# Kernel optimization log

Measured on AMD Instinct MI355X. Metric: run time of the kernel, lower is better.

Reference implementation:

```python
import jax, jax.numpy as jnp
import numpy as np

D_MODEL = 256
D_STATE = 16
D_CONV = 3
D_INNER = 256          # expand=1
D_HALF = D_INNER // 2  # 128
DT_RANK = 16           # ceil(256/16)
B, L0, L1 = 4, 4096, 4096


def setup_inputs() -> dict:
    key = jax.random.key(0)
    ks = jax.random.split(key, 10)
    u_0 = jax.random.normal(ks[0], (B, L0, D_MODEL), jnp.float32)
    u_1 = jax.random.normal(ks[1], (B, L1, D_MODEL), jnp.float32)
    in_proj_w = jax.random.normal(ks[2], (D_INNER, D_MODEL), jnp.float32) * (D_MODEL ** -0.5)
    conv_x_w = jax.random.normal(ks[3], (D_HALF, 1, D_CONV), jnp.float32) * (D_CONV ** -0.5)
    conv_z_w = jax.random.normal(ks[4], (D_HALF, 1, D_CONV), jnp.float32) * (D_CONV ** -0.5)
    x_proj_w = jax.random.normal(ks[5], (DT_RANK + 2 * D_STATE, D_HALF), jnp.float32) * (D_HALF ** -0.5)
    dt_init_std = DT_RANK ** -0.5
    dt_proj_w = jax.random.uniform(ks[6], (D_HALF, DT_RANK), jnp.float32, -dt_init_std, dt_init_std)
    # dt bias = inverse-softplus of dt ~ LogUniform(1e-3, 1e-1)
    dt = jnp.exp(jax.random.uniform(ks[7], (D_HALF,), jnp.float32) * (np.log(0.1) - np.log(0.001)) + np.log(0.001))
    dt = jnp.clip(dt, 1e-4, None)
    dt_proj_b = dt + jnp.log(-jnp.expm1(-dt))
    A_log = jnp.log(jnp.broadcast_to(jnp.arange(1, D_STATE + 1, dtype=jnp.float32), (D_HALF, D_STATE)))
    D_param = jnp.ones((D_HALF,), jnp.float32)
    out_proj_w = jax.random.normal(ks[8], (D_MODEL, D_INNER), jnp.float32) * (D_INNER ** -0.5)
    return {"u_0": u_0, "u_1": u_1, "in_proj_w": in_proj_w, "conv_x_w": conv_x_w,
            "conv_z_w": conv_z_w, "x_proj_w": x_proj_w, "dt_proj_w": dt_proj_w,
            "dt_proj_b": dt_proj_b, "A_log": A_log, "D": D_param, "out_proj_w": out_proj_w}


def _dwconv(x, w):
    # x: [B, C, L], w: [C, 1, K] depthwise, padding='same', no bias (conv_bias//2 == 0)
    return jax.lax.conv_general_dilated(
        x, w, window_strides=(1,), padding='SAME',
        feature_group_count=x.shape[1], dimension_numbers=('NCH', 'OIH', 'NCH'))


def _selective_scan(u, delta, A, Bm, Cm, Dv):
    # u, delta: [B, L, d]; A: [d, n]; Bm, Cm: [B, L, n]; Dv: [d]
    dA = jnp.exp(delta[..., None] * A)                       # [B, L, d, n]
    dBu = (delta * u)[..., None] * Bm[:, :, None, :]         # [B, L, d, n]
    def combine(c1, c2):
        a1, b1 = c1
        a2, b2 = c2
        return a2 * a1, a2 * b1 + b2
    _, h = jax.lax.associative_scan(combine, (dA, dBu), axis=1)  # h: [B, L, d, n]
    return jnp.einsum('bldn,bln->bld', h, Cm) + u * Dv


def _stream(u, in_proj_w, conv_x_w, conv_z_w, x_proj_w, dt_proj_w, dt_proj_b, A, D, out_proj_w):
    xz = jnp.einsum('bld,ed->ble', u, in_proj_w)             # [B, L, d_inner]
    x, z = jnp.split(xz, 2, axis=-1)                         # [B, L, d_half] each
    x = jnp.swapaxes(x, 1, 2)                                # [B, d_half, L]
    z = jnp.swapaxes(z, 1, 2)
    x_f = jax.nn.silu(_dwconv(x, conv_x_w))
    z_f = jax.nn.silu(_dwconv(z, conv_z_w))
    xf = jnp.swapaxes(x_f, 1, 2)                             # [B, L, d_half]
    dbl = jnp.einsum('bld,ed->ble', xf, x_proj_w)            # [B, L, dt_rank + 2n]
    dt, Bm, Cm = jnp.split(dbl, [DT_RANK, DT_RANK + D_STATE], axis=-1)
    dt = jnp.einsum('blr,dr->bld', dt, dt_proj_w)
    delta = jax.nn.softplus(dt + dt_proj_b)                  # delta_bias + delta_softplus
    y = _selective_scan(xf, delta, A, Bm, Cm, D)             # [B, L, d_half]
    cat = jnp.concatenate([y, jnp.swapaxes(z_f, 1, 2)], axis=-1)  # [B, L, d_inner]
    return jnp.einsum('ble,oe->blo', cat, out_proj_w)


def reference(u_0, u_1, in_proj_w, conv_x_w, conv_z_w, x_proj_w, dt_proj_w, dt_proj_b, A_log, D, out_proj_w):
    A = -jnp.exp(A_log)
    out0 = _stream(u_0, in_proj_w, conv_x_w, conv_z_w, x_proj_w, dt_proj_w, dt_proj_b, A, D, out_proj_w)
    out1 = _stream(u_1, in_proj_w, conv_x_w, conv_z_w, x_proj_w, dt_proj_w, dt_proj_b, A, D, out_proj_w)
    return (out0, out1)
```

## Files before the change

kernel.cpp:

```cpp
#include <hip/hip_runtime.h>
#include <hip/hip_bf16.h>
#include <cstdint>

#define DEV __device__ __forceinline__

typedef __attribute__((ext_vector_type(8))) short short8;
typedef __attribute__((ext_vector_type(4))) float f32x4;
typedef __attribute__((ext_vector_type(4))) unsigned short us4;
typedef __attribute__((ext_vector_type(8))) unsigned short us8;

DEV unsigned short f2bf(float x) {
    unsigned int u = __float_as_uint(x);
    unsigned int r = (u + 0x7FFFu + ((u >> 16) & 1u)) >> 16;
    return (unsigned short)r;
}
DEV float bf2f(unsigned short h) { return __uint_as_float(((unsigned int)h) << 16); }

DEV void gld_lds16(const unsigned short* g, unsigned short* l) {
    __builtin_amdgcn_global_load_lds(
        (const __attribute__((address_space(1))) unsigned int*)g,
        (__attribute__((address_space(3))) unsigned int*)l, 16, 0, 0);
}

#define LL 4096
#define DM 256
#define DH 128
#define SB_TOT 8
#define CH1 32
#define NCH 128
#define LOG2E 1.44269504088896f

__global__ __launch_bounds__(256) void prep_kernel(
    const float* __restrict__ u0, const float* __restrict__ u1,
    const float* __restrict__ inw, const float* __restrict__ outw,
    const float* __restrict__ xpw, const float* __restrict__ dtw,
    unsigned short* __restrict__ ubf, unsigned short* __restrict__ wbi,
    unsigned short* __restrict__ wbo, unsigned short* __restrict__ Wb)
{
    int gid = blockIdx.x * 256 + threadIdx.x;
    int i = gid * 4;
    if (i < 4194304) {
        f32x4 v = *(const f32x4*)&u0[i];
        us4 r = { f2bf(v.x), f2bf(v.y), f2bf(v.z), f2bf(v.w) };
        *(us4*)&ubf[i] = r;
    } else if (i < 8388608) {
        int j = i - 4194304;
        f32x4 v = *(const f32x4*)&u1[j];
        us4 r = { f2bf(v.x), f2bf(v.y), f2bf(v.z), f2bf(v.w) };
        *(us4*)&ubf[4194304 + j] = r;
    } else if (i < 8454144) {
        int j = i - 8388608;
        f32x4 v = *(const f32x4*)&inw[j];
        us4 r = { f2bf(v.x), f2bf(v.y), f2bf(v.z), f2bf(v.w) };
        *(us4*)&wbi[j] = r;
    } else if (i < 8519680) {
        int j = i - 8454144;
        f32x4 v = *(const f32x4*)&outw[j];
        us4 r = { f2bf(v.x), f2bf(v.y), f2bf(v.z), f2bf(v.w) };
        *(us4*)&wbo[j] = r;
    } else if (i < 8540160) {
        int j = i - 8519680;
        int n = j >> 7, k0 = j & 127;
        if (n < 128) {
            float a0 = 0.f, a1 = 0.f, a2 = 0.f, a3 = 0.f;
            const float* dw = dtw + n * 16;
            #pragma unroll
            for (int r = 0; r < 16; ++r) {
                float w = dw[r];
                const float* xr = xpw + r * 128 + k0;
                a0 = fmaf(w, xr[0], a0);
                a1 = fmaf(w, xr[1], a1);
                a2 = fmaf(w, xr[2], a2);
                a3 = fmaf(w, xr[3], a3);
            }
            us4 rr = { f2bf(a0), f2bf(a1), f2bf(a2), f2bf(a3) };
            *(us4*)&Wb[n * 128 + k0] = rr;
        } else {
            f32x4 v = *(const f32x4*)&xpw[(n - 112) * 128 + k0];
            us4 rr = { f2bf(v.x), f2bf(v.y), f2bf(v.z), f2bf(v.w) };
            *(us4*)&Wb[n * 128 + k0] = rr;
        }
    }
}

template<int F32OUT>
__global__ __launch_bounds__(256) void gemm_bt(
    const unsigned short* __restrict__ A, const unsigned short* __restrict__ B,
    float* __restrict__ Cf, unsigned short* __restrict__ Cb)
{
    __shared__ __align__(16) unsigned short As[128 * 32];
    __shared__ __align__(16) unsigned short Bs[128 * 32];
    const int t = threadIdx.x;
    const int m0 = blockIdx.x * 128, n0 = blockIdx.y * 128;
    const int lane = t & 63, wv = t >> 6;
    const int wm = (wv & 1) * 64, wn = (wv >> 1) * 64;
    const int lr = lane & 15, lk = (lane >> 4) * 8;
    const int srow = lane >> 2, scol = (lane & 3) * 8;

    f32x4 acc[4][4] = {};
    for (int kt = 0; kt < 8; ++kt) {
        const int k0 = kt * 32;
        #pragma unroll
        for (int h = 0; h < 2; ++h) {
            const int c = wv + h * 4;
            const unsigned short* ga = A + (size_t)(m0 + c * 16 + srow) * 256 + k0 + scol;
            const unsigned short* gb = B + (size_t)(n0 + c * 16 + srow) * 256 + k0 + scol;
            gld_lds16(ga, &As[c * 512]);
            gld_lds16(gb, &Bs[c * 512]);
        }
        __syncthreads();
        short8 av[4], bv[4];
        #pragma unroll
        for (int i = 0; i < 4; ++i) av[i] = *(const short8*)&As[(wm + i * 16 + lr) * 32 + lk];
        #pragma unroll
        for (int i = 0; i < 4; ++i) bv[i] = *(const short8*)&Bs[(wn + i * 16 + lr) * 32 + lk];
        #pragma unroll
        for (int i = 0; i < 4; ++i)
            #pragma unroll
            for (int j = 0; j < 4; ++j)
                acc[i][j] = __builtin_amdgcn_mfma_f32_16x16x32_bf16(av[i], bv[j], acc[i][j], 0, 0, 0);
        __syncthreads();
    }
    #pragma unroll
    for (int i = 0; i < 4; ++i) {
        #pragma unroll
        for (int j = 0; j < 4; ++j) {
            int r0 = m0 + wm + i * 16 + (lane >> 4) * 4;
            int cc = n0 + wn + j * 16 + lr;
            #pragma unroll
            for (int r = 0; r < 4; ++r) {
                float v = acc[i][j][r];
                if (F32OUT) Cf[(size_t)(r0 + r) * 256 + cc] = v;
                else        Cb[(size_t)(r0 + r) * 256 + cc] = f2bf(v);
            }
        }
    }
}

template<int FUSE_SCAN>
__global__ __launch_bounds__(256) void convproj_k(
    const unsigned short* __restrict__ xz, const unsigned short* __restrict__ Wb,
    const float* __restrict__ wx, const float* __restrict__ wz,
    const float* __restrict__ dtb, const float* __restrict__ alog,
    float* __restrict__ xf, unsigned short* __restrict__ catb,
    float* __restrict__ delta, float* __restrict__ BC,
    float* __restrict__ P, float* __restrict__ H)
{
    __shared__ __align__(16) unsigned short As[64 * 136];
    __shared__ float bc_s[64 * 16];
    const int t = threadIdx.x;
    const int m0 = blockIdx.x * 64;
    #pragma unroll
    for (int i = 0; i < 8; ++i) {
        int s = t + i * 256;
        int r = s >> 5, g = s & 31;
        int gr = m0 + r;
        int l = gr & 4095;
        int c; const float* wp; const unsigned short* bp;
        if (g < 16) { c = g * 8;        wp = wx; bp = xz + (size_t)gr * 256 + c; }
        else        { c = (g - 16) * 8; wp = wz; bp = xz + (size_t)gr * 256 + 128 + c; }
        us8 zz = (us8)0;
        us8 vm = (l > 0)    ? *(const us8*)(bp - 256) : zz;
        us8 v0 = *(const us8*)bp;
        us8 vp = (l < 4095) ? *(const us8*)(bp + 256) : zz;
        float o[8];
        #pragma unroll
        for (int j = 0; j < 8; ++j) {
            int cc = c + j;
            float v = bf2f(vm[j]) * wp[cc * 3] + bf2f(v0[j]) * wp[cc * 3 + 1]
                    + bf2f(vp[j]) * wp[cc * 3 + 2];
            v = v / (1.f + __expf(-v));
            o[j] = v;
        }
        us8 rb8 = { f2bf(o[0]), f2bf(o[1]), f2bf(o[2]), f2bf(o[3]),
                    f2bf(o[4]), f2bf(o[5]), f2bf(o[6]), f2bf(o[7]) };
        if (g < 16) {
            *(us8*)&As[r * 136 + c] = rb8;
            *(f32x4*)&xf[(size_t)gr * 128 + c]     = *(f32x4*)&o[0];
            *(f32x4*)&xf[(size_t)gr * 128 + c + 4] = *(f32x4*)&o[4];
        } else {
            *(us8*)&catb[(size_t)gr * 256 + 128 + c] = rb8;
        }
    }
    __syncthreads();
    const int lane = t & 63, wv = t >> 6;
    const int lr = lane & 15, lk = (lane >> 4) * 8;
    f32x4 acc[10] = {};
    #pragma unroll
    for (int kt = 0; kt < 4; ++kt) {
        const int k0 = kt * 32;
        short8 av = *(const short8*)&As[(wv * 16 + lr) * 136 + k0 + lk];
        #pragma unroll
        for (int j = 0; j < 10; ++j) {
            short8 bv = *(const short8*)(Wb + (j * 16 + lr) * 128 + k0 + lk);
            acc[j] = __builtin_amdgcn_mfma_f32_16x16x32_bf16(av, bv, acc[j], 0, 0, 0);
        }
    }
    const int r0 = (lane >> 4) * 4;
    #pragma unroll
    for (int j = 0; j < 10; ++j) {
        int col = j * 16 + lr;
        #pragma unroll
        for (int r = 0; r < 4; ++r) {
            float v = acc[j][r];
            int lrow = wv * 16 + r0 + r;
            size_t row = (size_t)m0 + lrow;
            if (j < 8) {
                float x = v + dtb[col];
                float sp = (x > 20.f) ? x : __logf(1.f + __expf(x));
                delta[row * 128 + col] = sp;
            } else {
                BC[row * 32 + (col - 128)] = v;
                if (FUSE_SCAN && j == 8) bc_s[lrow * 16 + lr] = v;
            }
        }
    }
    if (!FUSE_SCAN) return;

    __syncthreads();
    const int hh = t >> 7, tl = t & 127;
    const int sb = m0 >> 12;
    const int ch = ((m0 & 4095) >> 5) + hh;
    const size_t rb = (size_t)m0 + hh * 32;
    float Ar[16];
    #pragma unroll
    for (int n = 0; n < 16; ++n) Ar[n] = -__expf(alog[tl * 16 + n]) * LOG2E;
    float h[16], p[16];
    #pragma unroll
    for (int n = 0; n < 16; ++n) { h[n] = 0.f; p[n] = 1.f; }
    for (int i = 0; i < CH1; ++i) {
        float dt = delta[(rb + i) * DH + tl];
        float uu = xf[(rb + i) * DH + tl];
        float du = dt * uu;
        float bl[16];
        *(f32x4*)&bl[0]  = *(const f32x4*)&bc_s[(hh * 32 + i) * 16];
        *(f32x4*)&bl[4]  = *(const f32x4*)&bc_s[(hh * 32 + i) * 16 + 4];
        *(f32x4*)&bl[8]  = *(const f32x4*)&bc_s[(hh * 32 + i) * 16 + 8];
        *(f32x4*)&bl[12] = *(const f32x4*)&bc_s[(hh * 32 + i) * 16 + 12];
        #pragma unroll
        for (int n = 0; n < 16; ++n) {
            float a = exp2f(dt * Ar[n]);
            h[n] = fmaf(a, h[n], du * bl[n]);
            p[n] *= a;
        }
    }
    size_t ob = (((size_t)sb * NCH + ch) * 128 + tl) * 16;
    #pragma unroll
    for (int n4 = 0; n4 < 16; n4 += 4) {
        f32x4 pv = { p[n4], p[n4 + 1], p[n4 + 2], p[n4 + 3] };
        f32x4 hv = { h[n4], h[n4 + 1], h[n4 + 2], h[n4 + 3] };
        *(f32x4*)&P[ob + n4] = pv;
        *(f32x4*)&H[ob + n4] = hv;
    }
}

__global__ __launch_bounds__(128) void scan_p1(
    const float* __restrict__ delta, const float* __restrict__ xf,
    const float* __restrict__ BC, const float* __restrict__ alog,
    float* __restrict__ P, float* __restrict__ H)
{
    __shared__ float dt_s[CH1 * 128];
    __shared__ float du_s[CH1 * 128];
    __shared__ float b_s[CH1 * 16];
    int t = threadIdx.x;
    int ch = blockIdx.x, sb = blockIdx.y;
    size_t rb = (size_t)sb * LL + (size_t)ch * CH1;
    for (int q = t; q < CH1 * 32; q += 128) {
        int row = q >> 5, c4 = (q & 31) * 4;
        f32x4 dv = *(const f32x4*)&delta[(rb + row) * DH + c4];
        f32x4 uv = *(const f32x4*)&xf[(rb + row) * DH + c4];
        *(f32x4*)&dt_s[row * 128 + c4] = dv;
        f32x4 duv = dv * uv;
        *(f32x4*)&du_s[row * 128 + c4] = duv;
    }
    {
        int q = t & 127;
        int row = q >> 2, c4 = (q & 3) * 4;
        *(f32x4*)&b_s[row * 16 + c4] = *(const f32x4*)&BC[(rb + row) * 32 + c4];
    }
    __syncthreads();
    float Ar[16];
    #pragma unroll
    for (int n = 0; n < 16; ++n) Ar[n] = -__expf(alog[t * 16 + n]) * LOG2E;
    float h[16], p[16];
    #pragma unroll
    for (int n = 0; n < 16; ++n) { h[n] = 0.f; p[n] = 1.f; }
    for (int i = 0; i < CH1; ++i) {
        float dt = dt_s[i * 128 + t];
        float du = du_s[i * 128 + t];
        float bl[16];
        *(f32x4*)&bl[0]  = *(const f32x4*)&b_s[i * 16];
        *(f32x4*)&bl[4]  = *(const f32x4*)&b_s[i * 16 + 4];
        *(f32x4*)&bl[8]  = *(const f32x4*)&b_s[i * 16 + 8];
        *(f32x4*)&bl[12] = *(const f32x4*)&b_s[i * 16 + 12];
        #pragma unroll
        for (int n = 0; n < 16; ++n) {
            float a = exp2f(dt * Ar[n]);
            h[n] = fmaf(a, h[n], du * bl[n]);
            p[n] *= a;
        }
    }
    size_t ob = (((size_t)sb * NCH + ch) * 128 + t) * 16;
    #pragma unroll
    for (int n4 = 0; n4 < 16; n4 += 4) {
        f32x4 pv = { p[n4], p[n4 + 1], p[n4 + 2], p[n4 + 3] };
        f32x4 hv = { h[n4], h[n4 + 1], h[n4 + 2], h[n4 + 3] };
        *(f32x4*)&P[ob + n4] = pv;
        *(f32x4*)&H[ob + n4] = hv;
    }
}

__global__ __launch_bounds__(256) void scan_p2(const float* __restrict__ P, float* __restrict__ H)
{
    __shared__ float Ps[NCH * 16], Hs[NCH * 16];
    int t = threadIdx.x;
    int d = blockIdx.x, sb = blockIdx.y;
    for (int q = t; q < NCH * 4; q += 256) {
        int ch = q >> 2, c4 = (q & 3) * 4;
        size_t g = (((size_t)sb * NCH + ch) * 128 + d) * 16 + c4;
        *(f32x4*)&Ps[ch * 16 + c4] = *(const f32x4*)&P[g];
        *(f32x4*)&Hs[ch * 16 + c4] = *(const f32x4*)&H[g];
    }
    __syncthreads();
    if (t < 16) {
        float hin = 0.f;
        for (int c = 0; c < NCH; ++c) {
            float pp = Ps[c * 16 + t], hl = Hs[c * 16 + t];
            Hs[c * 16 + t] = hin;
            hin = fmaf(pp, hin, hl);
        }
    }
    __syncthreads();
    for (int q = t; q < NCH * 4; q += 256) {
        int ch = q >> 2, c4 = (q & 3) * 4;
        size_t g = (((size_t)sb * NCH + ch) * 128 + d) * 16 + c4;
        *(f32x4*)&H[g] = *(const f32x4*)&Hs[ch * 16 + c4];
    }
}

__global__ __launch_bounds__(128) void scan_p3(
    const float* __restrict__ delta, const float* __restrict__ xf,
    const float* __restrict__ BC, const float* __restrict__ alog,
    const float* __restrict__ Dp, const float* __restrict__ H,
    unsigned short* __restrict__ catb)
{
    __shared__ float dt_s[CH1 * 128];
    __shared__ float u_s[CH1 * 128];
    __shared__ float b_s[CH1 * 16];
    __shared__ float c_s[CH1 * 16];
    int t = threadIdx.x;
    int ch = blockIdx.x, sb = blockIdx.y;
    size_t rb = (size_t)sb * LL + (size_t)ch * CH1;
    for (int q = t; q < CH1 * 32; q += 128) {
        int row = q >> 5, c4 = (q & 31) * 4;
        *(f32x4*)&dt_s[row * 128 + c4] = *(const f32x4*)&delta[(rb + row) * DH + c4];
        *(f32x4*)&u_s[row * 128 + c4]  = *(const f32x4*)&xf[(rb + row) * DH + c4];
    }
    {
        int q = t & 127;
        int row = q >> 2, c4 = (q & 3) * 4;
        *(f32x4*)&b_s[row * 16 + c4] = *(const f32x4*)&BC[(rb + row) * 32 + c4];
        *(f32x4*)&c_s[row * 16 + c4] = *(const f32x4*)&BC[(rb + row) * 32 + 16 + c4];
    }
    __syncthreads();
    float Ar[16];
    #pragma unroll
    for (int n = 0; n < 16; ++n) Ar[n] = -__expf(alog[t * 16 + n]) * LOG2E;
    float Dv = Dp[t];
    size_t ob = (((size_t)sb * NCH + ch) * 128 + t) * 16;
    float h[16];
    #pragma unroll
    for (int n4 = 0; n4 < 16; n4 += 4) {
        f32x4 hv = *(const f32x4*)&H[ob + n4];
        h[n4] = hv.x; h[n4 + 1] = hv.y; h[n4 + 2] = hv.z; h[n4 + 3] = hv.w;
    }
    for (int i = 0; i < CH1; ++i) {
        float dt = dt_s[i * 128 + t];
        float uu = u_s[i * 128 + t];
        float du = dt * uu;
        float bl[16], cl[16];
        *(f32x4*)&bl[0]  = *(const f32x4*)&b_s[i * 16];
        *(f32x4*)&bl[4]  = *(const f32x4*)&b_s[i * 16 + 4];
        *(f32x4*)&bl[8]  = *(const f32x4*)&b_s[i * 16 + 8];
        *(f32x4*)&bl[12] = *(const f32x4*)&b_s[i * 16 + 12];
        *(f32x4*)&cl[0]  = *(const f32x4*)&c_s[i * 16];
        *(f32x4*)&cl[4]  = *(const f32x4*)&c_s[i * 16 + 4];
        *(f32x4*)&cl[8]  = *(const f32x4*)&c_s[i * 16 + 8];
        *(f32x4*)&cl[12] = *(const f32x4*)&c_s[i * 16 + 12];
        float y0 = uu * Dv, y1 = 0.f, y2 = 0.f, y3 = 0.f;
        #pragma unroll
        for (int n = 0; n < 16; n += 4) {
            float a0 = exp2f(dt * Ar[n]);
            float a1 = exp2f(dt * Ar[n + 1]);
            float a2 = exp2f(dt * Ar[n + 2]);
            float a3 = exp2f(dt * Ar[n + 3]);
            h[n]     = fmaf(a0, h[n],     du * bl[n]);
            h[n + 1] = fmaf(a1, h[n + 1], du * bl[n + 1]);
            h[n + 2] = fmaf(a2, h[n + 2], du * bl[n + 2]);
            h[n + 3] = fmaf(a3, h[n + 3], du * bl[n + 3]);
            y0 = fmaf(h[n],     cl[n],     y0);
            y1 = fmaf(h[n + 1], cl[n + 1], y1);
            y2 = fmaf(h[n + 2], cl[n + 2], y2);
            y3 = fmaf(h[n + 3], cl[n + 3], y3);
        }
        float y = (y0 + y1) + (y2 + y3);
        catb[(rb + i) * DM + t] = f2bf(y);
    }
}

extern "C" void kernel_launch(void* const* d_in, const int* in_sizes, int n_in,
                              void* d_out, int out_size, void* d_ws, size_t ws_size,
                              hipStream_t stream) {
    const float* u0   = (const float*)d_in[0];
    const float* u1   = (const float*)d_in[1];
    const float* inw  = (const float*)d_in[2];
    const float* cxw  = (const float*)d_in[3];
    const float* czw  = (const float*)d_in[4];
    const float* xpw  = (const float*)d_in[5];
    const float* dtw  = (const float*)d_in[6];
    const float* dtb  = (const float*)d_in[7];
    const float* alog = (const float*)d_in[8];
    const float* Dp   = (const float*)d_in[9];
    const float* outw = (const float*)d_in[10];

    char* ws = (char*)d_ws;
    unsigned short* ubf  = (unsigned short*)(ws + 0);
    float* delta         = (float*)(ws + 0);
    unsigned short* xzbf = (unsigned short*)(ws + 16777216);
    float* P_a           = (float*)(ws + 16777216);
    float* H_a           = (float*)(ws + 25165824);
    float* xf            = (float*)(ws + 33554432);
    float* BC            = (float*)(ws + 50331648);
    unsigned short* catb = (unsigned short*)(ws + 54525952);
    unsigned short* wbi  = (unsigned short*)(ws + 71303168);
    unsigned short* wbo  = (unsigned short*)(ws + 71434240);
    unsigned short* Wb   = (unsigned short*)(ws + 71565312);
    float* P_f           = (float*)(ws + 71606272);
    float* H_f           = (float*)(ws + 79994880);

    float* outp = (float*)d_out;

    prep_kernel<<<8340, 256, 0, stream>>>(u0, u1, inw, outw, xpw, dtw, ubf, wbi, wbo, Wb);
    gemm_bt<0><<<dim3(256, 2), 256, 0, stream>>>(ubf, wbi, nullptr, xzbf);

    if (ws_size >= 88383488ull) {
        convproj_k<1><<<512, 256, 0, stream>>>(xzbf, Wb, cxw, czw, dtb, alog,
                                               xf, catb, delta, BC, P_f, H_f);
        scan_p2<<<dim3(128, 8), 256, 0, stream>>>(P_f, H_f);
        scan_p3<<<dim3(NCH, 8), 128, 0, stream>>>(delta, xf, BC, alog, Dp, H_f, catb);
    } else {
        convproj_k<0><<<512, 256, 0, stream>>>(xzbf, Wb, cxw, czw, dtb, alog,
                                               xf, catb, delta, BC, nullptr, nullptr);
        scan_p1<<<dim3(NCH, 8), 128, 0, stream>>>(delta, xf, BC, alog, P_a, H_a);
        scan_p2<<<dim3(128, 8), 256, 0, stream>>>(P_a, H_a);
        scan_p3<<<dim3(NCH, 8), 128, 0, stream>>>(delta, xf, BC, alog, Dp, H_a, catb);
    }
    gemm_bt<1><<<dim3(256, 2), 256, 0, stream>>>(catb, wbo, outp, nullptr);
}
```

Measured before the change: 212.2 us.

## Halve convproj tile to 32 rows, split scan states across halves, drop LDS staging

convproj_k now handles 32 rows per block over 1024 blocks, with a remapped block-to-row order. The four waves split the 10 MFMA column tiles between two row tiles. In the fused scan, the two 128-thread halves now each own 8 of the 16 states for the same chunk instead of separate chunks, and delta for the chunk is preloaded into registers. scan_p1 and scan_p3 drop the LDS staging of delta and xf in favour of direct per-thread global loads plus a 32-entry register array. The aim is more parallelism and occupancy, less LDS use and shorter serial scan chains, at the cost of redundant delta/xf reads across halves and more register pressure.

```diff
diff --git a/kernel.cpp b/kernel.cpp
--- a/kernel.cpp
+++ b/kernel.cpp
@@ -146,12 +146,14 @@
     float* __restrict__ delta, float* __restrict__ BC,
     float* __restrict__ P, float* __restrict__ H)
 {
-    __shared__ __align__(16) unsigned short As[64 * 136];
-    __shared__ float bc_s[64 * 16];
+    __shared__ __align__(16) unsigned short As[32 * 136];
+    __shared__ float bc_s[32 * 16];
     const int t = threadIdx.x;
-    const int m0 = blockIdx.x * 64;
-    #pragma unroll
-    for (int i = 0; i < 8; ++i) {
+    const int kk = blockIdx.x & 7, yy = blockIdx.x >> 3;
+    const int m0 = (4 * kk + (yy & 3) + 32 * (yy >> 2)) * 32;
+
+    #pragma unroll
+    for (int i = 0; i < 4; ++i) {
         int s = t + i * 256;
         int r = s >> 5, g = s & 31;
         int gr = m0 + r;
@@ -185,33 +187,36 @@
     __syncthreads();
     const int lane = t & 63, wv = t >> 6;
     const int lr = lane & 15, lk = (lane >> 4) * 8;
-    f32x4 acc[10] = {};
+    const int rt = (wv & 1) * 16;
+    const int jbase = (wv >> 1) * 5;
+    f32x4 acc[5] = {};
     #pragma unroll
     for (int kt = 0; kt < 4; ++kt) {
         const int k0 = kt * 32;
-        short8 av = *(const short8*)&As[(wv * 16 + lr) * 136 + k0 + lk];
-        #pragma unroll
-        for (int j = 0; j < 10; ++j) {
-            short8 bv = *(const short8*)(Wb + (j * 16 + lr) * 128 + k0 + lk);
+        short8 av = *(const short8*)&As[(rt + lr) * 136 + k0 + lk];
+        #pragma unroll
+        for (int j = 0; j < 5; ++j) {
+            short8 bv = *(const short8*)(Wb + ((jbase + j) * 16 + lr) * 128 + k0 + lk);
             acc[j] = __builtin_amdgcn_mfma_f32_16x16x32_bf16(av, bv, acc[j], 0, 0, 0);
         }
     }
     const int r0 = (lane >> 4) * 4;
     #pragma unroll
-    for (int j = 0; j < 10; ++j) {
-        int col = j * 16 + lr;
+    for (int j = 0; j < 5; ++j) {
+        int jj = jbase + j;
+        int col = jj * 16 + lr;
         #pragma unroll
         for (int r = 0; r < 4; ++r) {
             float v = acc[j][r];
-            int lrow = wv * 16 + r0 + r;
+            int lrow = rt + r0 + r;
             size_t row = (size_t)m0 + lrow;
-            if (j < 8) {
+            if (jj < 8) {
                 float x = v + dtb[col];
                 float sp = (x > 20.f) ? x : __logf(1.f + __expf(x));
                 delta[row * 128 + col] = sp;
             } else {
                 BC[row * 32 + (col - 128)] = v;
-                if (FUSE_SCAN && j == 8) bc_s[lrow * 16 + lr] = v;
+                if (FUSE_SCAN && jj == 8) bc_s[lrow * 16 + lr] = v;
             }
         }
     }
@@ -220,38 +225,39 @@
     __syncthreads();
     const int hh = t >> 7, tl = t & 127;
     const int sb = m0 >> 12;
-    const int ch = ((m0 & 4095) >> 5) + hh;
-    const size_t rb = (size_t)m0 + hh * 32;
-    float Ar[16];
-    #pragma unroll
-    for (int n = 0; n < 16; ++n) Ar[n] = -__expf(alog[tl * 16 + n]) * LOG2E;
-    float h[16], p[16];
-    #pragma unroll
-    for (int n = 0; n < 16; ++n) { h[n] = 0.f; p[n] = 1.f; }
+    const int ch = (m0 & 4095) >> 5;
+    const size_t rb = (size_t)m0;
+    float dtr[32];
+    #pragma unroll
+    for (int i = 0; i < 32; ++i) dtr[i] = delta[(rb + i) * DH + tl];
+    float Ar[8];
+    #pragma unroll
+    for (int n = 0; n < 8; ++n) Ar[n] = -__expf(alog[tl * 16 + hh * 8 + n]) * LOG2E;
+    float h[8], p[8];
+    #pragma unroll
+    for (int n = 0; n < 8; ++n) { h[n] = 0.f; p[n] = 1.f; }
     for (int i = 0; i < CH1; ++i) {
-        float dt = delta[(rb + i) * DH + tl];
-        float uu = xf[(rb + i) * DH + tl];
-        float du = dt * uu;
-        float bl[16];
-        *(f32x4*)&bl[0]  = *(const f32x4*)&bc_s[(hh * 32 + i) * 16];
-        *(f32x4*)&bl[4]  = *(const f32x4*)&bc_s[(hh * 32 + i) * 16 + 4];
-        *(f32x4*)&bl[8]  = *(const f32x4*)&bc_s[(hh * 32 + i) * 16 + 8];
-        *(f32x4*)&bl[12] = *(const f32x4*)&bc_s[(hh * 32 + i) * 16 + 12];
-        #pragma unroll
-        for (int n = 0; n < 16; ++n) {
+        float dt = dtr[i];
+        float du = dt * xf[(rb + i) * DH + tl];
+        float bl[8];
+        *(f32x4*)&bl[0] = *(const f32x4*)&bc_s[i * 16 + hh * 8];
+        *(f32x4*)&bl[4] = *(const f32x4*)&bc_s[i * 16 + hh * 8 + 4];
+        #pragma unroll
+        for (int n = 0; n < 8; ++n) {
             float a = exp2f(dt * Ar[n]);
             h[n] = fmaf(a, h[n], du * bl[n]);
             p[n] *= a;
         }
     }
-    size_t ob = (((size_t)sb * NCH + ch) * 128 + tl) * 16;
-    #pragma unroll
-    for (int n4 = 0; n4 < 16; n4 += 4) {
-        f32x4 pv = { p[n4], p[n4 + 1], p[n4 + 2], p[n4 + 3] };
-        f32x4 hv = { h[n4], h[n4 + 1], h[n4 + 2], h[n4 + 3] };
-        *(f32x4*)&P[ob + n4] = pv;
-        *(f32x4*)&H[ob + n4] = hv;
-    }
+    size_t ob = (((size_t)sb * NCH + ch) * 128 + tl) * 16 + hh * 8;
+    f32x4 pv0 = { p[0], p[1], p[2], p[3] };
+    f32x4 pv1 = { p[4], p[5], p[6], p[7] };
+    f32x4 hv0 = { h[0], h[1], h[2], h[3] };
+    f32x4 hv1 = { h[4], h[5], h[6], h[7] };
+    *(f32x4*)&P[ob]     = pv0;
+    *(f32x4*)&P[ob + 4] = pv1;
+    *(f32x4*)&H[ob]     = hv0;
+    *(f32x4*)&H[ob + 4] = hv1;
 }
 
 __global__ __launch_bounds__(128) void scan_p1(
@@ -259,35 +265,27 @@
     const float* __restrict__ BC, const float* __restrict__ alog,
     float* __restrict__ P, float* __restrict__ H)
 {
-    __shared__ float dt_s[CH1 * 128];
-    __shared__ float du_s[CH1 * 128];
     __shared__ float b_s[CH1 * 16];
     int t = threadIdx.x;
     int ch = blockIdx.x, sb = blockIdx.y;
     size_t rb = (size_t)sb * LL + (size_t)ch * CH1;
-    for (int q = t; q < CH1 * 32; q += 128) {
-        int row = q >> 5, c4 = (q & 31) * 4;
-        f32x4 dv = *(const f32x4*)&delta[(rb + row) * DH + c4];
-        f32x4 uv = *(const f32x4*)&xf[(rb + row) * DH + c4];
-        *(f32x4*)&dt_s[row * 128 + c4] = dv;
-        f32x4 duv = dv * uv;
-        *(f32x4*)&du_s[row * 128 + c4] = duv;
-    }
     {
-        int q = t & 127;
-        int row = q >> 2, c4 = (q & 3) * 4;
+        int row = t >> 2, c4 = (t & 3) * 4;
         *(f32x4*)&b_s[row * 16 + c4] = *(const f32x4*)&BC[(rb + row) * 32 + c4];
     }
     __syncthreads();
     float Ar[16];
     #pragma unroll
     for (int n = 0; n < 16; ++n) Ar[n] = -__expf(alog[t * 16 + n]) * LOG2E;
+    float dtr[32];
+    #pragma unroll
+    for (int i = 0; i < 32; ++i) dtr[i] = delta[(rb + i) * DH + t];
     float h[16], p[16];
     #pragma unroll
     for (int n = 0; n < 16; ++n) { h[n] = 0.f; p[n] = 1.f; }
     for (int i = 0; i < CH1; ++i) {
-        float dt = dt_s[i * 128 + t];
-        float du = du_s[i * 128 + t];
+        float dt = dtr[i];
+        float du = dt * xf[(rb + i) * DH + t];
         float bl[16];
         *(f32x4*)&bl[0]  = *(const f32x4*)&b_s[i * 16];
         *(f32x4*)&bl[4]  = *(const f32x4*)&b_s[i * 16 + 4];
@@ -344,21 +342,13 @@
     const float* __restrict__ Dp, const float* __restrict__ H,
     unsigned short* __restrict__ catb)
 {
-    __shared__ float dt_s[CH1 * 128];
-    __shared__ float u_s[CH1 * 128];
     __shared__ float b_s[CH1 * 16];
     __shared__ float c_s[CH1 * 16];
     int t = threadIdx.x;
     int ch = blockIdx.x, sb = blockIdx.y;
     size_t rb = (size_t)sb * LL + (size_t)ch * CH1;
-    for (int q = t; q < CH1 * 32; q += 128) {
-        int row = q >> 5, c4 = (q & 31) * 4;
-        *(f32x4*)&dt_s[row * 128 + c4] = *(const f32x4*)&delta[(rb + row) * DH + c4];
-        *(f32x4*)&u_s[row * 128 + c4]  = *(const f32x4*)&xf[(rb + row) * DH + c4];
-    }
     {
-        int q = t & 127;
-        int row = q >> 2, c4 = (q & 3) * 4;
+        int row = t >> 2, c4 = (t & 3) * 4;
         *(f32x4*)&b_s[row * 16 + c4] = *(const f32x4*)&BC[(rb + row) * 32 + c4];
         *(f32x4*)&c_s[row * 16 + c4] = *(const f32x4*)&BC[(rb + row) * 32 + 16 + c4];
     }
@@ -367,6 +357,9 @@
     #pragma unroll
     for (int n = 0; n < 16; ++n) Ar[n] = -__expf(alog[t * 16 + n]) * LOG2E;
     float Dv = Dp[t];
+    float dtr[32];
+    #pragma unroll
+    for (int i = 0; i < 32; ++i) dtr[i] = delta[(rb + i) * DH + t];
     size_t ob = (((size_t)sb * NCH + ch) * 128 + t) * 16;
     float h[16];
     #pragma unroll
@@ -375,8 +368,8 @@
         h[n4] = hv.x; h[n4 + 1] = hv.y; h[n4 + 2] = hv.z; h[n4 + 3] = hv.w;
     }
     for (int i = 0; i < CH1; ++i) {
-        float dt = dt_s[i * 128 + t];
-        float uu = u_s[i * 128 + t];
+        float dt = dtr[i];
+        float uu = xf[(rb + i) * DH + t];
         float du = dt * uu;
         float bl[16], cl[16];
         *(f32x4*)&bl[0]  = *(const f32x4*)&b_s[i * 16];
@@ -444,13 +437,13 @@
     gemm_bt<0><<<dim3(256, 2), 256, 0, stream>>>(ubf, wbi, nullptr, xzbf);
 
     if (ws_size >= 88383488ull) {
-        convproj_k<1><<<512, 256, 0, stream>>>(xzbf, Wb, cxw, czw, dtb, alog,
-                                               xf, catb, delta, BC, P_f, H_f);
+        convproj_k<1><<<1024, 256, 0, stream>>>(xzbf, Wb, cxw, czw, dtb, alog,
+                                                xf, catb, delta, BC, P_f, H_f);
         scan_p2<<<dim3(128, 8), 256, 0, stream>>>(P_f, H_f);
         scan_p3<<<dim3(NCH, 8), 128, 0, stream>>>(delta, xf, BC, alog, Dp, H_f, catb);
     } else {
-        convproj_k<0><<<512, 256, 0, stream>>>(xzbf, Wb, cxw, czw, dtb, alog,
-                                               xf, catb, delta, BC, nullptr, nullptr);
+        convproj_k<0><<<1024, 256, 0, stream>>>(xzbf, Wb, cxw, czw, dtb, alog,
+                                                xf, catb, delta, BC, nullptr, nullptr);
         scan_p1<<<dim3(NCH, 8), 128, 0, stream>>>(delta, xf, BC, alog, P_a, H_a);
         scan_p2<<<dim3(128, 8), 256, 0, stream>>>(P_a, H_a);
         scan_p3<<<dim3(NCH, 8), 128, 0, stream>>>(delta, xf, BC, alog, Dp, H_a, catb);
```

Result: slower. 220.5 us (+3.9%).
